# Performance work log

Hardware: AMD Instinct MI355X
Metric: run time of the kernel (lower is better)

Reference implementation:

```python
import jax, jax.numpy as jnp
import numpy as np

HIDDEN = 128  # GL_Pair hidden_channels; premlp in_size = 2*HIDDEN = 256


def setup_inputs() -> dict:
    key = jax.random.key(0)
    ks = jax.random.split(key, 6)
    N = 1024
    pred_a = jax.random.normal(ks[0], (N, HIDDEN), dtype=jnp.float32)
    pred_b = jax.random.normal(ks[1], (N, HIDDEN), dtype=jnp.float32)
    # premlp: Linear(256 -> 256), ReLU, Linear(256 -> 1)
    W1 = jax.random.normal(ks[2], (2 * HIDDEN, 2 * HIDDEN), dtype=jnp.float32) * 0.0625
    b1 = jax.random.normal(ks[3], (2 * HIDDEN,), dtype=jnp.float32) * 0.01
    W2 = jax.random.normal(ks[4], (1, 2 * HIDDEN), dtype=jnp.float32) * 0.0625
    b2 = jax.random.normal(ks[5], (1,), dtype=jnp.float32) * 0.01
    return {"pred_a": pred_a, "pred_b": pred_b, "W1": W1, "b1": b1, "W2": W2, "b2": b2}


def reference(pred_a, pred_b, W1, b1, W2, b2):
    # Original loop: y_pred[m, j] = premlp(cat(pred_a[m], pred_b[j]))
    # Split W1 along its input dim: cat(a, b) @ W1.T == a @ W1[:, :H].T + b @ W1[:, H:].T
    ha = pred_a @ W1[:, :HIDDEN].T            # [N, 2H]
    hb = pred_b @ W1[:, HIDDEN:].T            # [N, 2H]
    h = jax.nn.relu(ha[:, None, :] + hb[None, :, :] + b1)  # [N, N, 2H]
    logits = jnp.einsum('mjk,k->mj', h, W2[0]) + b2[0]     # [N, N]
    return logits
```

## Files before the change

### kernel.cpp

```cpp
#include <hip/hip_runtime.h>

#define NN 1024
#define HH 128
#define KK 256

typedef float f32x2 __attribute__((ext_vector_type(2)));

__global__ __launch_bounds__(256) void prologue_kernel(
    const float* __restrict__ pred_a, const float* __restrict__ pred_b,
    const float* __restrict__ W1, const float* __restrict__ b1,
    float* __restrict__ HA, float* __restrict__ HBT)
{
    const int k = threadIdx.x;
    const int blk = blockIdx.x;
    const bool isB = blk >= 128;
    const int mbase = (isB ? blk - 128 : blk) * 8;
    const float* __restrict__ src = isB ? pred_b : pred_a;
    const float* __restrict__ wrow = W1 + k * KK + (isB ? HH : 0);

    float acc[8];
    const float init = isB ? 0.0f : b1[k];
    #pragma unroll
    for (int mm = 0; mm < 8; ++mm) acc[mm] = init;

    for (int i0 = 0; i0 < HH; i0 += 4) {
        const float4 w = *reinterpret_cast<const float4*>(wrow + i0);
        #pragma unroll
        for (int mm = 0; mm < 8; ++mm) {
            const float4 p = *reinterpret_cast<const float4*>(src + (mbase + mm) * HH + i0);
            float a = acc[mm];
            a = fmaf(p.x, w.x, a);
            a = fmaf(p.y, w.y, a);
            a = fmaf(p.z, w.z, a);
            a = fmaf(p.w, w.w, a);
            acc[mm] = a;
        }
    }

    if (!isB) {
        #pragma unroll
        for (int mm = 0; mm < 8; ++mm)
            HA[(mbase + mm) * KK + k] = acc[mm];
    } else {
        #pragma unroll
        for (int c = 0; c < 2; ++c) {
            float4 v = make_float4(acc[4*c+0], acc[4*c+1], acc[4*c+2], acc[4*c+3]);
            *reinterpret_cast<float4*>(HBT + k * NN + mbase + 4*c) = v;
        }
    }
}

__global__ __launch_bounds__(256, 2) void pair_kernel(
    const float* __restrict__ HA, const float* __restrict__ HBT,
    const float* __restrict__ W2, const float* __restrict__ b2,
    float* __restrict__ out)
{
    __shared__ float lds[KK * 64];
    const int t = threadIdx.x;
    const int lane = t & 63;
    const int wave = t >> 6;
    const int jbase = (blockIdx.x & 15) * 64;
    const int mbase = (blockIdx.x >> 4) * 32;

    #pragma unroll
    for (int c = 0; c < 64; ++c) {
        const int k = wave + c * 4;
        lds[k * 64 + lane] = HBT[k * NN + jbase + lane];
    }
    __syncthreads();

    const int m_w = __builtin_amdgcn_readfirstlane(mbase + wave * 8);
    const float* __restrict__ ha0 = HA + m_w * KK;

    f32x2 acc2[8];
    #pragma unroll
    for (int mm = 0; mm < 8; ++mm) { acc2[mm].x = 0.0f; acc2[mm].y = 0.0f; }

    #pragma unroll 4
    for (int k0 = 0; k0 < KK; k0 += 2) {
        f32x2 hb2;
        hb2.x = lds[k0 * 64 + lane];
        hb2.y = lds[(k0 + 1) * 64 + lane];
        const f32x2 w22 = *reinterpret_cast<const f32x2*>(W2 + k0);
        #pragma unroll
        for (int mm = 0; mm < 8; ++mm) {
            const f32x2 ha2 = *reinterpret_cast<const f32x2*>(ha0 + mm * KK + k0);
            f32x2 s2;
            asm("v_pk_add_f32 %0, %1, %2" : "=v"(s2) : "s"(ha2), "v"(hb2));
            s2.x = fmaxf(s2.x, 0.0f);
            s2.y = fmaxf(s2.y, 0.0f);
            asm("v_pk_fma_f32 %0, %1, %2, %0" : "+v"(acc2[mm]) : "v"(s2), "s"(w22));
        }
    }

    const float b2v = b2[0];
    #pragma unroll
    for (int mm = 0; mm < 8; ++mm)
        out[(m_w + mm) * NN + jbase + lane] = acc2[mm].x + acc2[mm].y + b2v;
}

extern "C" void kernel_launch(void* const* d_in, const int* in_sizes, int n_in,
                              void* d_out, int out_size, void* d_ws, size_t ws_size,
                              hipStream_t stream) {
    const float* pred_a = (const float*)d_in[0];
    const float* pred_b = (const float*)d_in[1];
    const float* W1     = (const float*)d_in[2];
    const float* b1     = (const float*)d_in[3];
    const float* W2     = (const float*)d_in[4];
    const float* b2     = (const float*)d_in[5];
    float* out = (float*)d_out;

    float* HA  = (float*)d_ws;
    float* HBT = HA + NN * KK;

    prologue_kernel<<<256, 256, 0, stream>>>(pred_a, pred_b, W1, b1, HA, HBT);
    pair_kernel<<<512, 256, 0, stream>>>(HA, HBT, W2, b2, out);
}
```

Baseline: 108.7 us.

## Stage HA and W2 in LDS with K-chunked tiles and smaller M-tiles

The pair kernel now splits K into two 128-wide chunks and stages HA rows, HBT columns and W2 into shared memory per chunk. HA is no longer read as scalar (SGPR) loads from global memory. The M tile per block is halved to 16 rows (4 per wave), which doubles the grid to 1024 blocks and raises the occupancy hint to 3 blocks. This trades scalar-load latency and heavy per-block LDS use for extra synchronisation, vector LDS reads of HA, and less register reuse per HB load.

Result: faster. 103.8 us (-4.5%).

```diff
diff --git a/kernel.cpp b/kernel.cpp
--- a/kernel.cpp
+++ b/kernel.cpp
@@ -50,53 +50,82 @@
     }
 }
 
-__global__ __launch_bounds__(256, 2) void pair_kernel(
+__global__ __launch_bounds__(256, 3) void pair_kernel(
     const float* __restrict__ HA, const float* __restrict__ HBT,
     const float* __restrict__ W2, const float* __restrict__ b2,
     float* __restrict__ out)
 {
-    __shared__ float lds[KK * 64];
+    __shared__ __align__(16) float lds[2048 + 8192 + 128];
+    float* lha = lds;
+    float* lhb = lds + 2048;
+    float* lw2 = lds + 2048 + 8192;
+
     const int t = threadIdx.x;
     const int lane = t & 63;
     const int wave = t >> 6;
     const int jbase = (blockIdx.x & 15) * 64;
-    const int mbase = (blockIdx.x >> 4) * 32;
+    const int mbase = (blockIdx.x >> 4) * 16;
+    const int wm = wave * 4;
 
+    f32x2 acc[4];
     #pragma unroll
-    for (int c = 0; c < 64; ++c) {
-        const int k = wave + c * 4;
-        lds[k * 64 + lane] = HBT[k * NN + jbase + lane];
-    }
-    __syncthreads();
+    for (int mm = 0; mm < 4; ++mm) { acc[mm].x = 0.0f; acc[mm].y = 0.0f; }
 
-    const int m_w = __builtin_amdgcn_readfirstlane(mbase + wave * 8);
-    const float* __restrict__ ha0 = HA + m_w * KK;
+    for (int kb = 0; kb < KK; kb += 128) {
+        if (kb) __syncthreads();
 
-    f32x2 acc2[8];
-    #pragma unroll
-    for (int mm = 0; mm < 8; ++mm) { acc2[mm].x = 0.0f; acc2[mm].y = 0.0f; }
+        #pragma unroll
+        for (int c = 0; c < 2; ++c) {
+            const int idx = c * 256 + t;
+            const int row = idx >> 5, col = (idx & 31) << 2;
+            *reinterpret_cast<float4*>(&lha[row * 128 + col]) =
+                *reinterpret_cast<const float4*>(&HA[(mbase + row) * KK + kb + col]);
+        }
+        #pragma unroll
+        for (int c = 0; c < 8; ++c) {
+            const int idx = c * 256 + t;
+            const int k = idx >> 4, col = (idx & 15) << 2;
+            *reinterpret_cast<float4*>(&lhb[k * 64 + col]) =
+                *reinterpret_cast<const float4*>(&HBT[(kb + k) * NN + jbase + col]);
+        }
+        if (t < 32)
+            *reinterpret_cast<float4*>(&lw2[t * 4]) =
+                *reinterpret_cast<const float4*>(&W2[kb + t * 4]);
+        __syncthreads();
 
-    #pragma unroll 4
-    for (int k0 = 0; k0 < KK; k0 += 2) {
-        f32x2 hb2;
-        hb2.x = lds[k0 * 64 + lane];
-        hb2.y = lds[(k0 + 1) * 64 + lane];
-        const f32x2 w22 = *reinterpret_cast<const f32x2*>(W2 + k0);
-        #pragma unroll
-        for (int mm = 0; mm < 8; ++mm) {
-            const f32x2 ha2 = *reinterpret_cast<const f32x2*>(ha0 + mm * KK + k0);
-            f32x2 s2;
-            asm("v_pk_add_f32 %0, %1, %2" : "=v"(s2) : "s"(ha2), "v"(hb2));
-            s2.x = fmaxf(s2.x, 0.0f);
-            s2.y = fmaxf(s2.y, 0.0f);
-            asm("v_pk_fma_f32 %0, %1, %2, %0" : "+v"(acc2[mm]) : "v"(s2), "s"(w22));
+        #pragma unroll 4
+        for (int k0 = 0; k0 < 128; k0 += 4) {
+            f32x2 hb01, hb23;
+            hb01.x = lhb[(k0 + 0) * 64 + lane];
+            hb01.y = lhb[(k0 + 1) * 64 + lane];
+            hb23.x = lhb[(k0 + 2) * 64 + lane];
+            hb23.y = lhb[(k0 + 3) * 64 + lane];
+            const float4 w4 = *reinterpret_cast<const float4*>(&lw2[k0]);
+            f32x2 w01; w01.x = w4.x; w01.y = w4.y;
+            f32x2 w23; w23.x = w4.z; w23.y = w4.w;
+            #pragma unroll
+            for (int mm = 0; mm < 4; ++mm) {
+                const float4 a4 = *reinterpret_cast<const float4*>(&lha[(wm + mm) * 128 + k0]);
+                f32x2 a01; a01.x = a4.x; a01.y = a4.y;
+                f32x2 a23; a23.x = a4.z; a23.y = a4.w;
+                f32x2 s;
+                asm("v_pk_add_f32 %0, %1, %2" : "=v"(s) : "v"(a01), "v"(hb01));
+                s.x = fmaxf(s.x, 0.0f);
+                s.y = fmaxf(s.y, 0.0f);
+                asm("v_pk_fma_f32 %0, %1, %2, %0" : "+v"(acc[mm]) : "v"(s), "v"(w01));
+                f32x2 r;
+                asm("v_pk_add_f32 %0, %1, %2" : "=v"(r) : "v"(a23), "v"(hb23));
+                r.x = fmaxf(r.x, 0.0f);
+                r.y = fmaxf(r.y, 0.0f);
+                asm("v_pk_fma_f32 %0, %1, %2, %0" : "+v"(acc[mm]) : "v"(r), "v"(w23));
+            }
         }
     }
 
     const float b2v = b2[0];
     #pragma unroll
-    for (int mm = 0; mm < 8; ++mm)
-        out[(m_w + mm) * NN + jbase + lane] = acc2[mm].x + acc2[mm].y + b2v;
+    for (int mm = 0; mm < 4; ++mm)
+        out[(mbase + wm + mm) * NN + jbase + lane] = acc[mm].x + acc[mm].y + b2v;
 }
 
 extern "C" void kernel_launch(void* const* d_in, const int* in_sizes, int n_in,
@@ -114,5 +143,5 @@
     float* HBT = HA + NN * KK;
 
     prologue_kernel<<<256, 256, 0, stream>>>(pred_a, pred_b, W1, b1, HA, HBT);
-    pair_kernel<<<512, 256, 0, stream>>>(HA, HBT, W2, b2, out);
+    pair_kernel<<<1024, 256, 0, stream>>>(HA, HBT, W2, b2, out);
 }
```
